# Kernel tuning notes

Hardware: AMD Instinct MI355X
Metric: run time of the kernel (lower is better)

## Reference

```python
import jax, jax.numpy as jnp
import numpy as np

NUM_HEADS = 16
HEAD_DIM = 128  # d_out // num_heads = 2048 // 16
THETA_BASE = 10000.0


def _rope_tables(seq_len, dtype):
    half = HEAD_DIM // 2
    inv_freq = 1.0 / THETA_BASE ** (jnp.arange(half, dtype=dtype) / half)
    pos = jnp.arange(seq_len, dtype=dtype)
    angles = pos[:, None] * inv_freq[None, :]            # [S, half]
    angles = jnp.concatenate([angles, angles], axis=-1)  # [S, HEAD_DIM]
    return jnp.cos(angles), jnp.sin(angles)


def _compute_rope(x, cos, sin):
    # x: [B, H, S, D]
    half = x.shape[-1] // 2
    x1, x2 = x[..., :half], x[..., half:]
    rotated = jnp.concatenate([-x2, x1], axis=-1)
    return x * cos[None, None] + rotated * sin[None, None]


def setup_inputs() -> dict:
    key = jax.random.key(0)
    k1, k2, k3 = jax.random.split(key, 3)
    B, S, D_IN, D_OUT = 2, 2048, 2048, 2048
    x = jax.random.normal(k1, (B, S, D_IN), dtype=jnp.float32)
    w_qkv = jax.random.normal(k2, (3 * D_OUT, D_IN), dtype=jnp.float32) * 0.02
    w_proj = jax.random.normal(k3, (D_OUT, D_OUT), dtype=jnp.float32) * 0.02
    return {"x": x, "w_qkv": w_qkv, "w_proj": w_proj}


def reference(x, w_qkv, w_proj):
    B, S, _ = x.shape
    # QKV projection (Linear with weight [3*d_out, d_in], no bias)
    qkv = jnp.einsum('bsd,ed->bse', x, w_qkv)                      # [B, S, 3*d_out]
    qkv = qkv.reshape(B, S, 3, NUM_HEADS, HEAD_DIM).transpose(2, 0, 3, 1, 4)
    q, k, v = qkv[0], qkv[1], qkv[2]                                # each [B, H, S, D]
    cos, sin = _rope_tables(S, x.dtype)
    q = _compute_rope(q, cos, sin)
    k = _compute_rope(k, cos, sin)
    scale = 1.0 / jnp.sqrt(jnp.asarray(HEAD_DIM, dtype=x.dtype))
    scores = jnp.einsum('bhqd,bhkd->bhqk', q, k) * scale            # [B, H, S, S]
    causal = jnp.tril(jnp.ones((S, S), dtype=bool))
    scores = jnp.where(causal[None, None], scores, jnp.finfo(scores.dtype).min)
    attn = jax.nn.softmax(scores, axis=-1)
    ctx = jnp.einsum('bhqk,bhkd->bhqd', attn, v)                    # [B, H, S, D]
    ctx = ctx.transpose(0, 2, 1, 3).reshape(B, S, NUM_HEADS * HEAD_DIM)
    return jnp.einsum('bsd,od->bso', ctx, w_proj)
```

## Files before the change

kernel.cpp:

```cpp
#include <hip/hip_runtime.h>
#include <hip/hip_bf16.h>
#include <math.h>

typedef unsigned short u16;
typedef __attribute__((ext_vector_type(8))) short bf16x8;
typedef __attribute__((ext_vector_type(4))) float f32x4;
typedef __attribute__((ext_vector_type(8))) unsigned short u16x8;

#define MFMA16(a, b, c) __builtin_amdgcn_mfma_f32_16x16x32_bf16(a, b, c, 0, 0, 0)
#define SWZ(o) ((o) ^ ((((o) >> 7) & 3) << 4))

__device__ __forceinline__ u16 f2bf(float f) {
  union { float f; unsigned u; } v; v.f = f;
  unsigned r = v.u + 0x7FFFu + ((v.u >> 16) & 1u);
  return (u16)(r >> 16);
}
__device__ __forceinline__ float bf2f(u16 h) {
  union { unsigned u; float f; } v; v.u = ((unsigned)h) << 16;
  return v.f;
}

__device__ __forceinline__ void gload_lds16(const void* g, void* l) {
  __builtin_amdgcn_global_load_lds((__attribute__((address_space(1))) void*)g,
                                   (__attribute__((address_space(3))) void*)l, 16, 0, 0);
}

__global__ void cast3(const float* __restrict__ a, const float* __restrict__ b,
                      const float* __restrict__ c, u16* __restrict__ oa,
                      u16* __restrict__ ob, u16* __restrict__ oc) {
  int i = blockIdx.x * 256 + threadIdx.x;
  int stride = gridDim.x * 256;
  for (; i < 6291456; i += stride) {
    const float4* src; uint2* dst; int j;
    if (i < 2097152)      { src = (const float4*)a; dst = (uint2*)oa; j = i; }
    else if (i < 5242880) { src = (const float4*)b; dst = (uint2*)ob; j = i - 2097152; }
    else                  { src = (const float4*)c; dst = (uint2*)oc; j = i - 5242880; }
    float4 v = src[j];
    unsigned lo = (unsigned)f2bf(v.x) | ((unsigned)f2bf(v.y) << 16);
    unsigned hi = (unsigned)f2bf(v.z) | ((unsigned)f2bf(v.w) << 16);
    dst[j] = make_uint2(lo, hi);
  }
}

__global__ void rope_table(float* __restrict__ tab) {
  int idx = blockIdx.x * 256 + threadIdx.x;
  int s = idx >> 6, j = idx & 63;
  double ang = (double)s * pow(10000.0, -(double)j / 64.0);
  tab[idx] = (float)cos(ang);
  tab[131072 + idx] = (float)sin(ang);
}

template<int EPI>
__global__ __launch_bounds__(512, 4) void gemm_r3(const u16* __restrict__ A, const u16* __restrict__ Bw,
                                                  void* __restrict__ C, void* __restrict__ C2,
                                                  const float* __restrict__ tab,
                                                  int M, int N, int K,
                                                  int xmBits, int cmMt, int cnNt) {
  __shared__ __align__(16) u16 shmem[36864];
  u16* Al = shmem;
  u16* Bl = shmem + 12288;
  const int t = threadIdx.x;
  const int w = t >> 6, l = t & 63;
  const int lr = l & 15, lg = l >> 4;
  const int wr = w >> 2, wc = w & 3;
  const int xcd = blockIdx.x & 7;
  const int loc = blockIdx.x >> 3;
  const int xm = xcd & ((1 << xmBits) - 1), xn = xcd >> xmBits;
  const int mt = xm * cmMt + (loc % cmMt);
  const int nt = xn * cnNt + (loc / cmMt);
  const int m0 = mt * 128, n0 = nt * 256;
  const int NT = K >> 5;

  const int pa = t * 16;
  const int oa = SWZ(pa);
  const u16* aSrc = A + (long)(m0 + (oa >> 6)) * K + ((oa & 63) >> 1);
  const int ob0 = SWZ(pa);
  const int ob1 = SWZ(8192 + pa);
  const u16* bSrc0 = Bw + (long)(n0 + (ob0 >> 6)) * K + ((ob0 & 63) >> 1);
  const u16* bSrc1 = Bw + (long)(n0 + ((ob1 - 8192) >> 6) + 128) * K + ((ob1 & 63) >> 1);
  const int ldsWave = w * 512;

  int aro[4], bro[4];
#pragma unroll
  for (int f = 0; f < 4; ++f) {
    int ab = (wr * 64 + f * 16 + lr) * 64 + lg * 16;
    aro[f] = SWZ(ab) >> 1;
    int bb = (wc * 64 + f * 16 + lr) * 64 + lg * 16;
    bro[f] = SWZ(bb) >> 1;
  }

  f32x4 acc[4][4];
#pragma unroll
  for (int i = 0; i < 4; ++i)
#pragma unroll
    for (int j = 0; j < 4; ++j)
#pragma unroll
      for (int e = 0; e < 4; ++e) acc[i][j][e] = 0.f;

#define STAGE(tt, sl)                                                     \
  do {                                                                    \
    gload_lds16(aSrc  + (tt) * 32, Al + (sl) * 4096 + ldsWave);           \
    gload_lds16(bSrc0 + (tt) * 32, Bl + (sl) * 8192 + ldsWave);           \
    gload_lds16(bSrc1 + (tt) * 32, Bl + (sl) * 8192 + 4096 + ldsWave);    \
  } while (0)

  STAGE(0, 0);
  STAGE(1, 1);
  asm volatile("s_waitcnt vmcnt(3)" ::: "memory");
  __builtin_amdgcn_s_barrier();

  int rs = 0, ss = 2;
  for (int tt = 0; tt < NT; ++tt) {
    const u16* as = Al + rs * 4096;
    const u16* bs = Bl + rs * 8192;
    bf16x8 b0 = *(const bf16x8*)(bs + bro[0]);
    bf16x8 b1 = *(const bf16x8*)(bs + bro[1]);
    bf16x8 b2 = *(const bf16x8*)(bs + bro[2]);
    bf16x8 b3 = *(const bf16x8*)(bs + bro[3]);
    bf16x8 a0 = *(const bf16x8*)(as + aro[0]);
    bf16x8 a1 = *(const bf16x8*)(as + aro[1]);
    bf16x8 a2 = *(const bf16x8*)(as + aro[2]);
    bf16x8 a3 = *(const bf16x8*)(as + aro[3]);
    if (tt + 2 < NT) STAGE(tt + 2, ss);
    __builtin_amdgcn_s_setprio(1);
    acc[0][0] = MFMA16(a0, b0, acc[0][0]);
    acc[0][1] = MFMA16(a0, b1, acc[0][1]);
    acc[0][2] = MFMA16(a0, b2, acc[0][2]);
    acc[0][3] = MFMA16(a0, b3, acc[0][3]);
    acc[1][0] = MFMA16(a1, b0, acc[1][0]);
    acc[1][1] = MFMA16(a1, b1, acc[1][1]);
    acc[1][2] = MFMA16(a1, b2, acc[1][2]);
    acc[1][3] = MFMA16(a1, b3, acc[1][3]);
    acc[2][0] = MFMA16(a2, b0, acc[2][0]);
    acc[2][1] = MFMA16(a2, b1, acc[2][1]);
    acc[2][2] = MFMA16(a2, b2, acc[2][2]);
    acc[2][3] = MFMA16(a2, b3, acc[2][3]);
    acc[3][0] = MFMA16(a3, b0, acc[3][0]);
    acc[3][1] = MFMA16(a3, b1, acc[3][1]);
    acc[3][2] = MFMA16(a3, b2, acc[3][2]);
    acc[3][3] = MFMA16(a3, b3, acc[3][3]);
    __builtin_amdgcn_s_setprio(0);
    asm volatile("s_waitcnt lgkmcnt(0)" ::: "memory");
    __builtin_amdgcn_sched_barrier(0);
    if (tt < NT - 2) asm volatile("s_waitcnt vmcnt(3)" ::: "memory");
    else             asm volatile("s_waitcnt vmcnt(0)" ::: "memory");
    __builtin_amdgcn_s_barrier();
    rs = (rs == 2) ? 0 : rs + 1;
    ss = (ss == 2) ? 0 : ss + 1;
  }
#undef STAGE

  if (EPI == 0) {
    float* Co = (float*)C;
#pragma unroll
    for (int mf = 0; mf < 4; ++mf)
#pragma unroll
      for (int nf = 0; nf < 4; ++nf)
#pragma unroll
        for (int j = 0; j < 4; ++j) {
          int row = m0 + wr * 64 + mf * 16 + lg * 4 + j;
          int col = n0 + wc * 64 + nf * 16 + lr;
          Co[(long)row * N + col] = acc[mf][nf][j];
        }
  } else {
    const int part = n0 >> 11;
    if (part < 2) {
#pragma unroll
      for (int mf = 0; mf < 4; ++mf)
#pragma unroll
        for (int nf = 0; nf < 4; ++nf) {
          ushort4 v;
          v.x = f2bf(acc[mf][nf][0]);
          v.y = f2bf(acc[mf][nf][1]);
          v.z = f2bf(acc[mf][nf][2]);
          v.w = f2bf(acc[mf][nf][3]);
          *(ushort4*)&shmem[((((w * 4 + mf) * 4 + nf) * 64) + l) * 4] = v;
        }
      __syncthreads();
      u16* Q = (u16*)C;
      const long PART = 8388608L;
      const float scale = (part == 0) ? 0.12751744906275268f : 1.0f;
      const int dlow = (wc & 1) == 0;
#pragma unroll
      for (int mf = 0; mf < 4; ++mf)
#pragma unroll
        for (int nf = 0; nf < 4; ++nf) {
          ushort4 pv = *(const ushort4*)&shmem[(((((w ^ 1) * 4 + mf) * 4 + nf) * 64) + l) * 4];
#pragma unroll
          for (int j = 0; j < 4; ++j) {
            int row = m0 + wr * 64 + mf * 16 + lg * 4 + j;
            int col = n0 + wc * 64 + nf * 16 + lr;
            int h = (col >> 7) & 15, d = col & 127;
            int b = row >> 11, s = row & 2047;
            int jj = d & 63;
            float cs = tab[s * 64 + jj];
            float sn = tab[131072 + s * 64 + jj];
            float own = acc[mf][nf][j];
            float oth = bf2f(((const u16*)&pv)[j]);
            float o = dlow ? (own * cs - oth * sn) : (own * cs + oth * sn);
            Q[part * PART + ((long)((b * 16 + h) * 2048 + s)) * 128 + d] = f2bf(o * scale);
          }
        }
    } else {
      u16* VT = (u16*)C2;
#pragma unroll
      for (int mf = 0; mf < 4; ++mf)
#pragma unroll
        for (int nf = 0; nf < 4; ++nf) {
          int row0 = m0 + wr * 64 + mf * 16 + lg * 4;
          int col = n0 + wc * 64 + nf * 16 + lr;
          int h = (col >> 7) & 15, d = col & 127;
          int b = row0 >> 11, s0 = row0 & 2047;
          ushort4 v;
          v.x = f2bf(acc[mf][nf][0]);
          v.y = f2bf(acc[mf][nf][1]);
          v.z = f2bf(acc[mf][nf][2]);
          v.w = f2bf(acc[mf][nf][3]);
          *(ushort4*)&VT[(long)(b * 16 + h) * 262144 + (long)d * 2048 + s0] = v;
        }
    }
  }
}

__global__ __launch_bounds__(256, 3) void flash_fwd(const u16* __restrict__ qg, const u16* __restrict__ kg,
                                                    const u16* __restrict__ vtg, u16* __restrict__ ctx) {
  const int bid = blockIdx.x;
  const int xcd = bid & 7;
  const int seq = bid >> 3;
  const int bh = xcd * 4 + (seq & 3);
  const int qi = 31 - (seq >> 2);
  const int t = threadIdx.x, w = t >> 6, l = t & 63;
  const int lr = l & 15, lg = l >> 4;
  const int q0 = qi * 64;
  const int nkv = qi + 1;
  const long skbase = (long)bh * 2048 * 128;
  const long vtbase = (long)bh * 128 * 2048;
  __shared__ __align__(16) u16 Kl[64 * 128];
  __shared__ __align__(16) u16 Vl[128 * 64];
  __shared__ __align__(16) u16 Pl[4][16][72];

  bf16x8 qf[4];
  {
    const u16* qrow = qg + skbase + (long)(q0 + w * 16 + lr) * 128;
#pragma unroll
    for (int dc = 0; dc < 4; ++dc) qf[dc] = *(const bf16x8*)(qrow + dc * 32 + lg * 8);
  }
  f32x4 acc[8];
#pragma unroll
  for (int dc = 0; dc < 8; ++dc)
#pragma unroll
    for (int e = 0; e < 4; ++e) acc[dc][e] = 0.f;
  float mrow[4] = {-1e30f, -1e30f, -1e30f, -1e30f};
  float lsum[4] = {0.f, 0.f, 0.f, 0.f};

  const u16* kga = kg + skbase + (long)(t >> 4) * 128 + (t & 15) * 8;
  const u16* vga = vtg + vtbase + (long)(t >> 3) * 2048 + (t & 7) * 8;
  const int kWrO = (t >> 4) * 256 + (((t & 15) * 16) ^ (((t >> 4) & 7) << 4));
  const int vWrO = (t >> 3) * 128 + (((t & 7) * 16) ^ (((t >> 3) & 7) << 4));
  const int msk = (lr & 7) << 4;
  char* KlB = (char*)Kl;
  char* VlB = (char*)Vl;

  u16x8 rk[4], rv[4];
#pragma unroll
  for (int it = 0; it < 4; ++it) {
    rk[it] = *(const u16x8*)(kga + it * 2048);
    rv[it] = *(const u16x8*)(vga + it * 65536);
  }

  for (int kvt = 0; kvt < nkv; ++kvt) {
    __syncthreads();
#pragma unroll
    for (int it = 0; it < 4; ++it) {
      *(u16x8*)(KlB + kWrO + it * 4096) = rk[it];
      *(u16x8*)(VlB + vWrO + it * 4096) = rv[it];
    }
    __syncthreads();
    if (kvt + 1 < nkv) {
      const u16* ka = kga + (long)(kvt + 1) * 8192;
      const u16* va = vga + (long)(kvt + 1) * 64;
#pragma unroll
      for (int it = 0; it < 4; ++it) {
        rk[it] = *(const u16x8*)(ka + it * 2048);
        rv[it] = *(const u16x8*)(va + it * 65536);
      }
    }

    const int kv0 = kvt * 64;
    f32x4 sc[4];
#pragma unroll
    for (int c = 0; c < 4; ++c)
#pragma unroll
      for (int e = 0; e < 4; ++e) sc[c][e] = 0.f;
    __builtin_amdgcn_s_setprio(1);
#pragma unroll
    for (int dc = 0; dc < 4; ++dc)
#pragma unroll
      for (int c = 0; c < 4; ++c) {
        bf16x8 kf = *(const bf16x8*)(KlB + c * 4096 + lr * 256 + ((dc * 64 + lg * 16) ^ msk));
        sc[c] = MFMA16(qf[dc], kf, sc[c]);
      }
    __builtin_amdgcn_s_setprio(0);

    if (kvt == qi) {
#pragma unroll
      for (int c = 0; c < 4; ++c)
#pragma unroll
        for (int j = 0; j < 4; ++j) {
          int kvi = kv0 + c * 16 + lr;
          int qq = q0 + w * 16 + lg * 4 + j;
          if (kvi > qq) sc[c][j] = -1e30f;
        }
    }

    float pmax[4];
#pragma unroll
    for (int j = 0; j < 4; ++j)
      pmax[j] = fmaxf(fmaxf(sc[0][j], sc[1][j]), fmaxf(sc[2][j], sc[3][j]));
#pragma unroll
    for (int off = 8; off >= 1; off >>= 1)
#pragma unroll
      for (int j = 0; j < 4; ++j)
        pmax[j] = fmaxf(pmax[j], __shfl_xor(pmax[j], off));

    int skip = __all(pmax[0] <= mrow[0] + 8.f && pmax[1] <= mrow[1] + 8.f &&
                     pmax[2] <= mrow[2] + 8.f && pmax[3] <= mrow[3] + 8.f);
    if (!skip) {
#pragma unroll
      for (int j = 0; j < 4; ++j) {
        float mn = fmaxf(mrow[j], pmax[j]);
        float alpha = __builtin_amdgcn_exp2f(mrow[j] - mn);
        mrow[j] = mn;
        lsum[j] *= alpha;
#pragma unroll
        for (int dc = 0; dc < 8; ++dc) acc[dc][j] *= alpha;
      }
    }

    float rsum[4] = {0.f, 0.f, 0.f, 0.f};
#pragma unroll
    for (int c = 0; c < 4; ++c)
#pragma unroll
      for (int j = 0; j < 4; ++j) {
        float p = __builtin_amdgcn_exp2f(sc[c][j] - mrow[j]);
        sc[c][j] = p;
        rsum[j] += p;
      }
#pragma unroll
    for (int off = 8; off >= 1; off >>= 1)
#pragma unroll
      for (int j = 0; j < 4; ++j)
        rsum[j] += __shfl_xor(rsum[j], off);
#pragma unroll
    for (int j = 0; j < 4; ++j) lsum[j] += rsum[j];

#pragma unroll
    for (int c = 0; c < 4; ++c)
#pragma unroll
      for (int j = 0; j < 4; ++j)
        Pl[w][lg * 4 + j][c * 16 + lr] = f2bf(sc[c][j]);

    __builtin_amdgcn_s_setprio(1);
#pragma unroll
    for (int kc = 0; kc < 2; ++kc) {
      bf16x8 pa = *(const bf16x8*)&Pl[w][lr][kc * 32 + lg * 8];
#pragma unroll
      for (int dc = 0; dc < 8; ++dc) {
        bf16x8 vb = *(const bf16x8*)(VlB + dc * 2048 + lr * 128 + ((kc * 64 + lg * 16) ^ msk));
        acc[dc] = MFMA16(pa, vb, acc[dc]);
      }
    }
    __builtin_amdgcn_s_setprio(0);
  }

  const int b = bh >> 4, h = bh & 15;
#pragma unroll
  for (int j = 0; j < 4; ++j) {
    float inv = 1.f / lsum[j];
    int s = q0 + w * 16 + lg * 4 + j;
    u16* orow = ctx + ((long)(b * 2048 + s)) * 2048 + h * 128;
#pragma unroll
    for (int dc = 0; dc < 8; ++dc)
      orow[dc * 16 + lr] = f2bf(acc[dc][j] * inv);
  }
}

extern "C" void kernel_launch(void* const* d_in, const int* in_sizes, int n_in,
                              void* d_out, int out_size, void* d_ws, size_t ws_size,
                              hipStream_t stream) {
  const float* x = (const float*)d_in[0];
  const float* wqkv = (const float*)d_in[1];
  const float* wproj = (const float*)d_in[2];
  float* out = (float*)d_out;

  u16* xb   = (u16*)d_ws;
  u16* wqb  = xb + 8388608;
  u16* wpb  = wqb + 12582912;
  u16* qkv  = wpb + 4194304;
  u16* vt   = qkv + 25165824;
  u16* ctx  = vt + 8388608;
  float* tab = (float*)(ctx + 8388608);

  cast3<<<4096, 256, 0, stream>>>(x, wqkv, wproj, xb, wqb, wpb);
  rope_table<<<512, 256, 0, stream>>>(tab);

  gemm_r3<1><<<768, 512, 0, stream>>>(xb, wqb, qkv, vt, tab, 4096, 6144, 2048, 1, 16, 6);

  flash_fwd<<<1024, 256, 0, stream>>>(qkv, qkv + 8388608, vt, ctx);

  gemm_r3<0><<<256, 512, 0, stream>>>(ctx, wpb, out, nullptr, nullptr, 4096, 2048, 2048, 2, 8, 4);
}
```

Before: 271.4 us.

## Add dedicated 256x256-tile QKV GEMM with double-buffered 64-wide K stages

Replaces the templated 128x256 GEMM used for the QKV projection with a new kernel using 256x256 output tiles, K-step 64, double-buffered LDS staging via global_load_lds, and interleaved LDS reads with MFMA groups. The aim is more arithmetic per byte loaded and fewer blocks (384 instead of 768), cutting global/LDS traffic per flop. The output projection keeps the old kernel, now specialised to the fp32 epilogue. The cost is heavier register use (128 accumulators per thread, occupancy 2) and 128KB of LDS, which may limit latency hiding and leave CUs idle with only 384 blocks on the device.

```diff
diff --git a/kernel.cpp b/kernel.cpp
--- a/kernel.cpp
+++ b/kernel.cpp
@@ -50,11 +50,188 @@
   tab[131072 + idx] = (float)sin(ang);
 }
 
-template<int EPI>
+__global__ __launch_bounds__(512, 2) void gemm_qkv(const u16* __restrict__ A, const u16* __restrict__ Bw,
+                                                   u16* __restrict__ Q, u16* __restrict__ VT,
+                                                   const float* __restrict__ tab,
+                                                   int M, int N, int K) {
+  __shared__ __align__(16) u16 lds[65536];
+  const int t = threadIdx.x, w = t >> 6, l = t & 63;
+  const int lr = l & 15, lg = l >> 4;
+  const int wr = w >> 2, wc = w & 3;
+  const int xcd = blockIdx.x & 7, loc = blockIdx.x >> 3;
+  const int mt = (xcd & 1) * 8 + (loc % 8);
+  const int nt = (xcd >> 1) * 6 + (loc / 8);
+  const int m0 = mt * 256, n0 = nt * 256;
+  const int NT = K >> 6;
+
+  const int srow = t >> 3;
+  const int so = ((t & 7) * 16) ^ ((srow & 7) << 4);
+  const u16* aS = A + (long)(m0 + srow) * K + (so >> 1);
+  const u16* bS = Bw + (long)(n0 + srow) * K + (so >> 1);
+  char* ldsB = (char*)lds;
+  const int dA = t * 16;
+
+  const int msk = (lr & 7) << 4;
+  const int sw0 = (lg * 16) ^ msk;
+  const int aRd = (wr * 128 + lr) * 128 + sw0;
+  const int bRd = 32768 + (wc * 64 + lr) * 128 + sw0;
+
+  f32x4 acc[8][4];
+#pragma unroll
+  for (int i = 0; i < 8; ++i)
+#pragma unroll
+    for (int j = 0; j < 4; ++j)
+#pragma unroll
+      for (int e = 0; e < 4; ++e) acc[i][j][e] = 0.f;
+
+#define STGA(tt, buf)                                                   \
+  do { _Pragma("unroll")                                                \
+    for (int i = 0; i < 4; ++i)                                         \
+      gload_lds16(aS + (long)i * 64 * K + (tt) * 64,                    \
+                  ldsB + (buf) * 65536 + i * 8192 + dA); } while (0)
+#define STGB(tt, buf)                                                   \
+  do { _Pragma("unroll")                                                \
+    for (int i = 0; i < 4; ++i)                                         \
+      gload_lds16(bS + (long)i * 64 * K + (tt) * 64,                    \
+                  ldsB + (buf) * 65536 + 32768 + i * 8192 + dA); } while (0)
+
+  STGA(0, 0); STGB(0, 0);
+  STGA(1, 1); STGB(1, 1);
+  asm volatile("s_waitcnt vmcnt(8)" ::: "memory");
+  __builtin_amdgcn_s_barrier();
+
+  for (int tt = 0; tt < NT; ++tt) {
+    char* base = ldsB + (tt & 1) * 65536;
+    bf16x8 af[4][2], bf[4][2];
+#pragma unroll
+    for (int nf = 0; nf < 2; ++nf)
+#pragma unroll
+      for (int kk = 0; kk < 2; ++kk)
+        bf[nf][kk] = *(const bf16x8*)(base + ((bRd + nf * 2048) ^ (kk * 64)));
+#pragma unroll
+    for (int mf = 0; mf < 4; ++mf)
+#pragma unroll
+      for (int kk = 0; kk < 2; ++kk)
+        af[mf][kk] = *(const bf16x8*)(base + ((aRd + mf * 2048) ^ (kk * 64)));
+    asm volatile("s_waitcnt lgkmcnt(0)" ::: "memory");
+    __builtin_amdgcn_sched_barrier(0);
+    __builtin_amdgcn_s_setprio(1);
+#pragma unroll
+    for (int mf = 0; mf < 4; ++mf)
+#pragma unroll
+      for (int nf = 0; nf < 2; ++nf)
+#pragma unroll
+        for (int kk = 0; kk < 2; ++kk)
+          acc[mf][nf] = MFMA16(af[mf][kk], bf[nf][kk], acc[mf][nf]);
+    __builtin_amdgcn_s_setprio(0);
+#pragma unroll
+    for (int nf = 2; nf < 4; ++nf)
+#pragma unroll
+      for (int kk = 0; kk < 2; ++kk)
+        bf[nf][kk] = *(const bf16x8*)(base + ((bRd + nf * 2048) ^ (kk * 64)));
+    asm volatile("s_waitcnt lgkmcnt(0)" ::: "memory");
+    __builtin_amdgcn_sched_barrier(0);
+    __builtin_amdgcn_s_setprio(1);
+#pragma unroll
+    for (int mf = 0; mf < 4; ++mf)
+#pragma unroll
+      for (int nf = 2; nf < 4; ++nf)
+#pragma unroll
+        for (int kk = 0; kk < 2; ++kk)
+          acc[mf][nf] = MFMA16(af[mf][kk], bf[nf][kk], acc[mf][nf]);
+    __builtin_amdgcn_s_setprio(0);
+#pragma unroll
+    for (int mf = 0; mf < 4; ++mf)
+#pragma unroll
+      for (int kk = 0; kk < 2; ++kk)
+        af[mf][kk] = *(const bf16x8*)(base + ((aRd + (mf + 4) * 2048) ^ (kk * 64)));
+    asm volatile("s_waitcnt lgkmcnt(0)" ::: "memory");
+    __builtin_amdgcn_sched_barrier(0);
+    __builtin_amdgcn_s_barrier();
+    __builtin_amdgcn_s_setprio(1);
+#pragma unroll
+    for (int mf = 0; mf < 4; ++mf)
+#pragma unroll
+      for (int nf = 0; nf < 2; ++nf)
+#pragma unroll
+        for (int kk = 0; kk < 2; ++kk)
+          acc[mf + 4][nf] = MFMA16(af[mf][kk], bf[nf][kk], acc[mf + 4][nf]);
+    __builtin_amdgcn_s_setprio(0);
+    if (tt + 2 < NT) { STGA(tt + 2, tt & 1); STGB(tt + 2, tt & 1); }
+    __builtin_amdgcn_s_setprio(1);
+#pragma unroll
+    for (int mf = 0; mf < 4; ++mf)
+#pragma unroll
+      for (int nf = 2; nf < 4; ++nf)
+#pragma unroll
+        for (int kk = 0; kk < 2; ++kk)
+          acc[mf + 4][nf] = MFMA16(af[mf][kk], bf[nf][kk], acc[mf + 4][nf]);
+    __builtin_amdgcn_s_setprio(0);
+    if (tt + 3 < NT) asm volatile("s_waitcnt vmcnt(8)" ::: "memory");
+    else             asm volatile("s_waitcnt vmcnt(0)" ::: "memory");
+    __builtin_amdgcn_s_barrier();
+  }
+#undef STGA
+#undef STGB
+
+  const int part = n0 >> 11;
+  if (part < 2) {
+#pragma unroll
+    for (int mf = 0; mf < 8; ++mf)
+#pragma unroll
+      for (int nf = 0; nf < 4; ++nf) {
+        ushort4 v;
+        v.x = f2bf(acc[mf][nf][0]);
+        v.y = f2bf(acc[mf][nf][1]);
+        v.z = f2bf(acc[mf][nf][2]);
+        v.w = f2bf(acc[mf][nf][3]);
+        *(ushort4*)&lds[((((w * 8 + mf) * 4 + nf) * 64) + l) * 4] = v;
+      }
+    __syncthreads();
+    const long PART = 8388608L;
+    const float scale = (part == 0) ? 0.12751744906275268f : 1.0f;
+    const int dlow = (wc & 1) == 0;
+#pragma unroll
+    for (int mf = 0; mf < 8; ++mf)
+#pragma unroll
+      for (int nf = 0; nf < 4; ++nf) {
+        ushort4 pv = *(const ushort4*)&lds[(((((w ^ 1) * 8 + mf) * 4 + nf) * 64) + l) * 4];
+#pragma unroll
+        for (int j = 0; j < 4; ++j) {
+          int row = m0 + wr * 128 + mf * 16 + lg * 4 + j;
+          int col = n0 + wc * 64 + nf * 16 + lr;
+          int h = (col >> 7) & 15, d = col & 127;
+          int b = row >> 11, s = row & 2047;
+          int jj = d & 63;
+          float cs = tab[s * 64 + jj];
+          float sn = tab[131072 + s * 64 + jj];
+          float own = acc[mf][nf][j];
+          float oth = bf2f(((const u16*)&pv)[j]);
+          float o = dlow ? (own * cs - oth * sn) : (own * cs + oth * sn);
+          Q[part * PART + ((long)((b * 16 + h) * 2048 + s)) * 128 + d] = f2bf(o * scale);
+        }
+      }
+  } else {
+#pragma unroll
+    for (int mf = 0; mf < 8; ++mf)
+#pragma unroll
+      for (int nf = 0; nf < 4; ++nf) {
+        int row0 = m0 + wr * 128 + mf * 16 + lg * 4;
+        int col = n0 + wc * 64 + nf * 16 + lr;
+        int h = (col >> 7) & 15, d = col & 127;
+        int b = row0 >> 11, s0 = row0 & 2047;
+        ushort4 v;
+        v.x = f2bf(acc[mf][nf][0]);
+        v.y = f2bf(acc[mf][nf][1]);
+        v.z = f2bf(acc[mf][nf][2]);
+        v.w = f2bf(acc[mf][nf][3]);
+        *(ushort4*)&VT[(long)(b * 16 + h) * 262144 + (long)d * 2048 + s0] = v;
+      }
+  }
+}
+
 __global__ __launch_bounds__(512, 4) void gemm_r3(const u16* __restrict__ A, const u16* __restrict__ Bw,
-                                                  void* __restrict__ C, void* __restrict__ C2,
-                                                  const float* __restrict__ tab,
-                                                  int M, int N, int K,
+                                                  float* __restrict__ C, int M, int N, int K,
                                                   int xmBits, int cmMt, int cnNt) {
   __shared__ __align__(16) u16 shmem[36864];
   u16* Al = shmem;
@@ -150,76 +327,16 @@
   }
 #undef STAGE
 
-  if (EPI == 0) {
-    float* Co = (float*)C;
-#pragma unroll
-    for (int mf = 0; mf < 4; ++mf)
-#pragma unroll
-      for (int nf = 0; nf < 4; ++nf)
-#pragma unroll
-        for (int j = 0; j < 4; ++j) {
-          int row = m0 + wr * 64 + mf * 16 + lg * 4 + j;
-          int col = n0 + wc * 64 + nf * 16 + lr;
-          Co[(long)row * N + col] = acc[mf][nf][j];
-        }
-  } else {
-    const int part = n0 >> 11;
-    if (part < 2) {
-#pragma unroll
-      for (int mf = 0; mf < 4; ++mf)
-#pragma unroll
-        for (int nf = 0; nf < 4; ++nf) {
-          ushort4 v;
-          v.x = f2bf(acc[mf][nf][0]);
-          v.y = f2bf(acc[mf][nf][1]);
-          v.z = f2bf(acc[mf][nf][2]);
-          v.w = f2bf(acc[mf][nf][3]);
-          *(ushort4*)&shmem[((((w * 4 + mf) * 4 + nf) * 64) + l) * 4] = v;
-        }
-      __syncthreads();
-      u16* Q = (u16*)C;
-      const long PART = 8388608L;
-      const float scale = (part == 0) ? 0.12751744906275268f : 1.0f;
-      const int dlow = (wc & 1) == 0;
-#pragma unroll
-      for (int mf = 0; mf < 4; ++mf)
-#pragma unroll
-        for (int nf = 0; nf < 4; ++nf) {
-          ushort4 pv = *(const ushort4*)&shmem[(((((w ^ 1) * 4 + mf) * 4 + nf) * 64) + l) * 4];
-#pragma unroll
-          for (int j = 0; j < 4; ++j) {
-            int row = m0 + wr * 64 + mf * 16 + lg * 4 + j;
-            int col = n0 + wc * 64 + nf * 16 + lr;
-            int h = (col >> 7) & 15, d = col & 127;
-            int b = row >> 11, s = row & 2047;
-            int jj = d & 63;
-            float cs = tab[s * 64 + jj];
-            float sn = tab[131072 + s * 64 + jj];
-            float own = acc[mf][nf][j];
-            float oth = bf2f(((const u16*)&pv)[j]);
-            float o = dlow ? (own * cs - oth * sn) : (own * cs + oth * sn);
-            Q[part * PART + ((long)((b * 16 + h) * 2048 + s)) * 128 + d] = f2bf(o * scale);
-          }
-        }
-    } else {
-      u16* VT = (u16*)C2;
-#pragma unroll
-      for (int mf = 0; mf < 4; ++mf)
-#pragma unroll
-        for (int nf = 0; nf < 4; ++nf) {
-          int row0 = m0 + wr * 64 + mf * 16 + lg * 4;
-          int col = n0 + wc * 64 + nf * 16 + lr;
-          int h = (col >> 7) & 15, d = col & 127;
-          int b = row0 >> 11, s0 = row0 & 2047;
-          ushort4 v;
-          v.x = f2bf(acc[mf][nf][0]);
-          v.y = f2bf(acc[mf][nf][1]);
-          v.z = f2bf(acc[mf][nf][2]);
-          v.w = f2bf(acc[mf][nf][3]);
-          *(ushort4*)&VT[(long)(b * 16 + h) * 262144 + (long)d * 2048 + s0] = v;
-        }
-    }
-  }
+#pragma unroll
+  for (int mf = 0; mf < 4; ++mf)
+#pragma unroll
+    for (int nf = 0; nf < 4; ++nf)
+#pragma unroll
+      for (int j = 0; j < 4; ++j) {
+        int row = m0 + wr * 64 + mf * 16 + lg * 4 + j;
+        int col = n0 + wc * 64 + nf * 16 + lr;
+        C[(long)row * N + col] = acc[mf][nf][j];
+      }
 }
 
 __global__ __launch_bounds__(256, 3) void flash_fwd(const u16* __restrict__ qg, const u16* __restrict__ kg,
@@ -404,9 +521,9 @@
   cast3<<<4096, 256, 0, stream>>>(x, wqkv, wproj, xb, wqb, wpb);
   rope_table<<<512, 256, 0, stream>>>(tab);
 
-  gemm_r3<1><<<768, 512, 0, stream>>>(xb, wqb, qkv, vt, tab, 4096, 6144, 2048, 1, 16, 6);
+  gemm_qkv<<<384, 512, 0, stream>>>(xb, wqb, qkv, vt, tab, 4096, 6144, 2048);
 
   flash_fwd<<<1024, 256, 0, stream>>>(qkv, qkv + 8388608, vt, ctx);
 
-  gemm_r3<0><<<256, 512, 0, stream>>>(ctx, wpb, out, nullptr, nullptr, 4096, 2048, 2048, 2, 8, 4);
-}
+  gemm_r3<<<256, 512, 0, stream>>>(ctx, wpb, out, 4096, 2048, 2048, 2, 8, 4);
+}
```

Result: no change. 276.1 us (+1.7%).

## Load K and V fragments directly from global memory in flash attention

Applied to the files above, without the earlier changes.

Removes the shared-memory staging of K and V tiles, along with the register prefetch and both block barriers per KV tile. Each wave now reads its MFMA operand fragments straight from global memory, relying on L2/L1 caching for the reuse across the four waves. This cuts LDS traffic and synchronisation but gives up the explicit prefetch overlap, and it multiplies global load requests by four because every wave fetches the same K/V data.

```diff
diff --git a/kernel.cpp b/kernel.cpp
--- a/kernel.cpp
+++ b/kernel.cpp
@@ -235,8 +235,6 @@
   const int nkv = qi + 1;
   const long skbase = (long)bh * 2048 * 128;
   const long vtbase = (long)bh * 128 * 2048;
-  __shared__ __align__(16) u16 Kl[64 * 128];
-  __shared__ __align__(16) u16 Vl[128 * 64];
   __shared__ __align__(16) u16 Pl[4][16][72];
 
   bf16x8 qf[4];
@@ -253,54 +251,31 @@
   float mrow[4] = {-1e30f, -1e30f, -1e30f, -1e30f};
   float lsum[4] = {0.f, 0.f, 0.f, 0.f};
 
-  const u16* kga = kg + skbase + (long)(t >> 4) * 128 + (t & 15) * 8;
-  const u16* vga = vtg + vtbase + (long)(t >> 3) * 2048 + (t & 7) * 8;
-  const int kWrO = (t >> 4) * 256 + (((t & 15) * 16) ^ (((t >> 4) & 7) << 4));
-  const int vWrO = (t >> 3) * 128 + (((t & 7) * 16) ^ (((t >> 3) & 7) << 4));
-  const int msk = (lr & 7) << 4;
-  char* KlB = (char*)Kl;
-  char* VlB = (char*)Vl;
-
-  u16x8 rk[4], rv[4];
-#pragma unroll
-  for (int it = 0; it < 4; ++it) {
-    rk[it] = *(const u16x8*)(kga + it * 2048);
-    rv[it] = *(const u16x8*)(vga + it * 65536);
-  }
+  const u16* kfb = kg + skbase + (long)lr * 128 + lg * 8;
+  const u16* vfb = vtg + vtbase + (long)lr * 2048 + lg * 8;
 
   for (int kvt = 0; kvt < nkv; ++kvt) {
-    __syncthreads();
-#pragma unroll
-    for (int it = 0; it < 4; ++it) {
-      *(u16x8*)(KlB + kWrO + it * 4096) = rk[it];
-      *(u16x8*)(VlB + vWrO + it * 4096) = rv[it];
-    }
-    __syncthreads();
-    if (kvt + 1 < nkv) {
-      const u16* ka = kga + (long)(kvt + 1) * 8192;
-      const u16* va = vga + (long)(kvt + 1) * 64;
-#pragma unroll
-      for (int it = 0; it < 4; ++it) {
-        rk[it] = *(const u16x8*)(ka + it * 2048);
-        rv[it] = *(const u16x8*)(va + it * 65536);
-      }
-    }
-
     const int kv0 = kvt * 64;
     f32x4 sc[4];
 #pragma unroll
     for (int c = 0; c < 4; ++c)
 #pragma unroll
       for (int e = 0; e < 4; ++e) sc[c][e] = 0.f;
-    __builtin_amdgcn_s_setprio(1);
-#pragma unroll
-    for (int dc = 0; dc < 4; ++dc)
-#pragma unroll
-      for (int c = 0; c < 4; ++c) {
-        bf16x8 kf = *(const bf16x8*)(KlB + c * 4096 + lr * 256 + ((dc * 64 + lg * 16) ^ msk));
-        sc[c] = MFMA16(qf[dc], kf, sc[c]);
-      }
-    __builtin_amdgcn_s_setprio(0);
+
+#pragma unroll
+    for (int c = 0; c < 4; ++c) {
+      const u16* kr = kfb + (long)(kv0 + c * 16) * 128;
+      bf16x8 kf0 = *(const bf16x8*)(kr);
+      bf16x8 kf1 = *(const bf16x8*)(kr + 32);
+      bf16x8 kf2 = *(const bf16x8*)(kr + 64);
+      bf16x8 kf3 = *(const bf16x8*)(kr + 96);
+      __builtin_amdgcn_s_setprio(1);
+      sc[c] = MFMA16(qf[0], kf0, sc[c]);
+      sc[c] = MFMA16(qf[1], kf1, sc[c]);
+      sc[c] = MFMA16(qf[2], kf2, sc[c]);
+      sc[c] = MFMA16(qf[3], kf3, sc[c]);
+      __builtin_amdgcn_s_setprio(0);
+    }
 
     if (kvt == qi) {
 #pragma unroll
@@ -360,17 +335,18 @@
       for (int j = 0; j < 4; ++j)
         Pl[w][lg * 4 + j][c * 16 + lr] = f2bf(sc[c][j]);
 
-    __builtin_amdgcn_s_setprio(1);
 #pragma unroll
     for (int kc = 0; kc < 2; ++kc) {
       bf16x8 pa = *(const bf16x8*)&Pl[w][lr][kc * 32 + lg * 8];
+      const u16* vr = vfb + kv0 + kc * 32;
+      __builtin_amdgcn_s_setprio(1);
 #pragma unroll
       for (int dc = 0; dc < 8; ++dc) {
-        bf16x8 vb = *(const bf16x8*)(VlB + dc * 2048 + lr * 128 + ((kc * 64 + lg * 16) ^ msk));
+        bf16x8 vb = *(const bf16x8*)(vr + (long)(dc * 16) * 2048);
         acc[dc] = MFMA16(pa, vb, acc[dc]);
       }
-    }
-    __builtin_amdgcn_s_setprio(0);
+      __builtin_amdgcn_s_setprio(0);
+    }
   }
 
   const int b = bh >> 4, h = bh & 15;
```

New measurement: 455.5 us. +67.8%, slower.
